# Kernel optimization log

Hardware: AMD Instinct MI355X
Metric: run time of the kernel (lower is better)

## Reference

```python
import jax, jax.numpy as jnp
import numpy as np
import math

# init kwargs (constants)
HSHIFT, VSHIFT, ANGLE = 2, 2, 2
BS, C, H, W = 2048, 1, 64, 64


def setup_inputs() -> dict:
    key = jax.random.key(0)
    k1, k2 = jax.random.split(key)
    fm1 = jax.random.normal(k1, (BS, C, H, W), dtype=jnp.float32)
    fm2 = jax.random.normal(k2, (BS, C, H, W), dtype=jnp.float32)
    return {"fm1": fm1, "fm2": fm2}


def _warp_rotate(img, theta_deg, h, w):
    """Equivalent of cv2.warpAffine(img, cv2.getRotationMatrix2D((w/2,h/2), theta, 1)).

    img: [bs, h, w]. Bilinear interpolation, constant-0 border.
    Returns (rotated_img [bs,h,w], rotated_ones_mask [h,w]).
    cv2 inverts the forward map internally; inverse of rotation by theta about
    the center is rotation by -theta about the center.
    """
    t = -theta_deg * (math.pi / 180.0)
    alpha = jnp.cos(t)
    beta = jnp.sin(t)
    cx, cy = w / 2.0, h / 2.0
    ys, xs = jnp.meshgrid(jnp.arange(h, dtype=jnp.float32),
                          jnp.arange(w, dtype=jnp.float32), indexing="ij")
    x_src = alpha * xs + beta * ys + (1.0 - alpha) * cx - beta * cy
    y_src = -beta * xs + alpha * ys + beta * cx + (1.0 - alpha) * cy

    x0 = jnp.floor(x_src)
    y0 = jnp.floor(y_src)
    wx = x_src - x0
    wy = y_src - y0
    x0i = x0.astype(jnp.int32)
    y0i = y0.astype(jnp.int32)

    out = jnp.zeros_like(img)
    msk = jnp.zeros((h, w), img.dtype)
    corners = ((0, 0, (1 - wy) * (1 - wx)), (0, 1, (1 - wy) * wx),
               (1, 0, wy * (1 - wx)), (1, 1, wy * wx))
    for dy, dx, wgt in corners:
        yi = y0i + dy
        xi = x0i + dx
        valid = ((yi >= 0) & (yi < h) & (xi >= 0) & (xi < w)).astype(img.dtype)
        yc = jnp.clip(yi, 0, h - 1)
        xc = jnp.clip(xi, 0, w - 1)
        out = out + (wgt * valid) * img[:, yc, xc]
        msk = msk + wgt * valid
    return out, msk


def _forward(fm1, fm2):
    bs, c, h, w = fm1.shape
    thetas = jnp.arange(-ANGLE, ANGLE + 1, dtype=jnp.float32)
    min_dist = jnp.full((bs,), jnp.finfo(jnp.float32).max, dtype=jnp.float32)
    for bh in range(-HSHIFT, HSHIFT + 1):
        for bv in range(-VSHIFT, VSHIFT + 1):
            if bh >= 0:
                r1, r2 = fm1[:, :, :, :w - bh], fm2[:, :, :, bh:]
            else:
                r1, r2 = fm1[:, :, :, -bh:], fm2[:, :, :, :w + bh]
            if bv >= 0:
                r1, r2 = r1[:, :, :h - bv, :], r2[:, :, bv:, :]
            else:
                r1, r2 = r1[:, :, -bv:, :], r2[:, :, :h + bv, :]
            oh, ow = r1.shape[2], r1.shape[3]
            r1s = r1[:, 0]  # [bs, oh, ow] (C==1)
            # original detaches ref2 before warping (cv2 path)
            r2s = jax.lax.stop_gradient(r2[:, 0])

            def one_theta(theta, r1s=r1s, r2s=r2s, oh=oh, ow=ow):
                rr2, mk = _warp_rotate(r2s, theta, oh, ow)
                se = ((r1s - rr2) ** 2) * mk  # [bs, oh, ow]
                return se.reshape(se.shape[0], -1).sum(1) / mk.sum()

            dists = jax.vmap(one_theta)(thetas)  # [ntheta, bs]
            min_dist = jnp.minimum(min_dist, dists.min(0))
    return min_dist


def reference(fm1, fm2):
    return _forward(fm1, fm2)
```

## Files before the change

kernel.cpp:

```cpp
#include <hip/hip_runtime.h>
#include <hip/hip_fp16.h>
#include <math.h>

#define NTH 5
#define GLO 66
#define GHI 132
#define PS (GLO + 4096 + GHI)

#define ALP0 0.99939082701909576f
#define ALP1 0.99984769515639127f
constexpr float ALPc[5] = {ALP0, ALP1, 1.0f, ALP1, ALP0};
constexpr float BETc[5] = {0.03489949670250097f, 0.01745240643728351f, 0.0f,
                           -0.01745240643728351f, -0.03489949670250097f};

__device__ __forceinline__ unsigned h2bits(float a, float b) {
    __half2 h = __floats2half2_rn(a, b);
    return *(unsigned*)&h;
}
__device__ __forceinline__ __half2 h2(unsigned u) { return *(__half2*)&u; }

__device__ __forceinline__ int pkadd(int a, int b) {
    __half2 r = __hadd2(*(__half2*)&a, *(__half2*)&b);
    return *(int*)&r;
}
__device__ __forceinline__ int hred16(__half2 v) {
    int x = *(int*)&v;
    int t = __builtin_amdgcn_update_dpp(0, x, 0xB1, 0xF, 0xF, true);
    x = pkadd(x, t);
    t = __builtin_amdgcn_update_dpp(0, x, 0x4E, 0xF, 0xF, true);
    x = pkadd(x, t);
    t = __builtin_amdgcn_update_dpp(0, x, 0x141, 0xF, 0xF, true);
    x = pkadd(x, t);
    t = __builtin_amdgcn_update_dpp(0, x, 0x140, 0xF, 0xF, true);
    x = pkadd(x, t);
    return x;
}

__global__ void pack_kernel(const float* __restrict__ fm1,
                            const float* __restrict__ fm2,
                            __half* __restrict__ fm1h,
                            __half* __restrict__ fm2h) {
    const int g = blockIdx.x >> 1;
    const int half = blockIdx.x & 1;
    const int tid = threadIdx.x;
    const size_t inb = (size_t)g * 16 * 4096;
    #pragma unroll
    for (int i = 0; i < 2; i++) {
        const int p = half * 2048 + tid + 1024 * i;
        uint4 wa, wb, va, vb;
        wa.x = h2bits(fm1[inb + 0 * 4096 + p], fm1[inb + 1 * 4096 + p]);
        wa.y = h2bits(fm1[inb + 2 * 4096 + p], fm1[inb + 3 * 4096 + p]);
        wa.z = h2bits(fm1[inb + 4 * 4096 + p], fm1[inb + 5 * 4096 + p]);
        wa.w = h2bits(fm1[inb + 6 * 4096 + p], fm1[inb + 7 * 4096 + p]);
        wb.x = h2bits(fm1[inb + 8 * 4096 + p], fm1[inb + 9 * 4096 + p]);
        wb.y = h2bits(fm1[inb + 10 * 4096 + p], fm1[inb + 11 * 4096 + p]);
        wb.z = h2bits(fm1[inb + 12 * 4096 + p], fm1[inb + 13 * 4096 + p]);
        wb.w = h2bits(fm1[inb + 14 * 4096 + p], fm1[inb + 15 * 4096 + p]);
        va.x = h2bits(fm2[inb + 0 * 4096 + p], fm2[inb + 1 * 4096 + p]);
        va.y = h2bits(fm2[inb + 2 * 4096 + p], fm2[inb + 3 * 4096 + p]);
        va.z = h2bits(fm2[inb + 4 * 4096 + p], fm2[inb + 5 * 4096 + p]);
        va.w = h2bits(fm2[inb + 6 * 4096 + p], fm2[inb + 7 * 4096 + p]);
        vb.x = h2bits(fm2[inb + 8 * 4096 + p], fm2[inb + 9 * 4096 + p]);
        vb.y = h2bits(fm2[inb + 10 * 4096 + p], fm2[inb + 11 * 4096 + p]);
        vb.z = h2bits(fm2[inb + 12 * 4096 + p], fm2[inb + 13 * 4096 + p]);
        vb.w = h2bits(fm2[inb + 14 * 4096 + p], fm2[inb + 15 * 4096 + p]);
        *(uint4*)(fm1h + ((size_t)(g * 2 + 0) * 4096 + p) * 8) = wa;
        *(uint4*)(fm1h + ((size_t)(g * 2 + 1) * 4096 + p) * 8) = wb;
        *(uint4*)(fm2h + ((size_t)(g * 2 + 0) * 4096 + p) * 8) = va;
        *(uint4*)(fm2h + ((size_t)(g * 2 + 1) * 4096 + p) * 8) = vb;
    }
}

__global__ void table_kernel(uint4* __restrict__ tab, float* __restrict__ denom) {
    const int bid = blockIdx.x;
    const int s = bid >> 2, tj = bid & 3;
    const int ti = tj < 2 ? tj : tj + 1;
    const int tid = threadIdx.x;
    const int bh = (s / 5) - 2;
    const int bv = (s % 5) - 2;
    const int ox2 = bh >= 0 ? bh : 0;
    const int ow = 64 - (bh >= 0 ? bh : -bh);
    const int oy2 = bv >= 0 ? bv : 0;
    const int oh = 64 - (bv >= 0 ? bv : -bv);
    const float cx = 0.5f * (float)ow;
    const float cy = 0.5f * (float)oh;
    const float alpha = ALPc[ti], beta = BETc[ti];
    __shared__ float mred[4];
    float macc = 0.0f;
    for (int i = 0; i < 16; i++) {
        const int px = tid + 256 * i;
        const int y = px >> 6, x = px & 63;
        uint4 e = make_uint4(0u, 0u, 0u, (unsigned)GLO);
        if (x < ow && y < oh) {
            const float xs = (float)x, yf = (float)y;
            const float hx = fmaf(alpha, xs, (1.0f - alpha) * cx - beta * cy);
            const float hy = fmaf(-beta, xs, beta * cx + (1.0f - alpha) * cy);
            const float xsrc = fmaf(beta, yf, hx);
            const float ysrc = fmaf(alpha, yf, hy);
            const float x0f = floorf(xsrc), y0f = floorf(ysrc);
            const float wx = xsrc - x0f, wy = ysrc - y0f;
            const int x0 = (int)x0f, y0 = (int)y0f;
            const float ax0 = ((unsigned)x0 < (unsigned)ow) ? (1.f - wx) : 0.f;
            const float ax1 = ((unsigned)(x0 + 1) < (unsigned)ow) ? wx : 0.f;
            const float ay0 = ((unsigned)y0 < (unsigned)oh) ? (1.f - wy) : 0.f;
            const float ay1 = ((unsigned)(y0 + 1) < (unsigned)oh) ? wy : 0.f;
            const int x0c = min(max(x0, -1), ow - 1);
            const int y0c = min(max(y0, -1), oh - 1);
            const float mk = (ax0 + ax1) * (ay0 + ay1);
            e.x = h2bits(ay0 * ax0, ay0 * ax1);
            e.y = h2bits(ay1 * ax0, ay1 * ax1);
            e.z = h2bits(mk, 0.0f);
            e.w = (unsigned)(GLO + (y0c + oy2) * 64 + (x0c + ox2));
            macc += mk;
        }
        tab[(size_t)bid * 4096 + px] = e;
    }
    #pragma unroll
    for (int off = 32; off; off >>= 1) macc += __shfl_xor(macc, off);
    if ((tid & 63) == 0) mred[tid >> 6] = macc;
    __syncthreads();
    if (tid == 0) {
        denom[s * 5 + ti] = mred[0] + mred[1] + mred[2] + mred[3];
        if (tj == 0) denom[s * 5 + 2] = (float)(ow * oh);
    }
}

__launch_bounds__(1024, 8)
__global__ void wrsl_main(const __half* __restrict__ fm1h,
                          const __half* __restrict__ fm2h,
                          const uint4* __restrict__ tab,
                          const float* __restrict__ denom,
                          float* __restrict__ out) {
    __shared__ uint4 lds[PS];
    __shared__ float redm[16][4][40];
    __shared__ float colsum[40];

    const int tid = threadIdx.x;
    const int g = blockIdx.x & 127;
    const int pl = (blockIdx.x >> 7) & 1;
    const int hf = (blockIdx.x >> 8) & 1;
    const int sBeg = hf ? 13 : 0;
    const int sEnd = hf ? 25 : 13;
    const size_t pbase = (size_t)(g * 2 + pl) * 4096;

    {
        const uint4* src = (const uint4*)(fm2h + pbase * 8);
        #pragma unroll
        for (int i = 0; i < 4; i++)
            lds[GLO + tid + 1024 * i] = src[tid + 1024 * i];
        if (tid < GLO + GHI) {
            const int off = (tid < GLO) ? tid : (4096 + tid);
            lds[off] = make_uint4(0u, 0u, 0u, 0u);
        }
    }
    const int lane = tid & 63, wid = tid >> 6;
    __syncthreads();

    float best = 3.4028234663852886e38f;

    for (int s = sBeg; s < sEnd; s++) {
        const int bh = (s / 5) - 2;
        const int bv = (s % 5) - 2;
        const int ox1 = bh >= 0 ? 0 : -bh;
        const int ox2 = bh >= 0 ? bh : 0;
        const int ow = 64 - (bh >= 0 ? bh : -bh);
        const int oy1 = bv >= 0 ? 0 : -bv;
        const int oy2 = bv >= 0 ? bv : 0;
        const int oh = 64 - (bv >= 0 ? bv : -bv);
        const int xcap = ox1 + min(lane, ow - 1);

        uint4 nr[4];
        #pragma unroll
        for (int k = 0; k < 4; k++) {
            const int p1 = (oy1 + min(wid + 16 * k, oh - 1)) * 64 + xcap;
            uint4 a = *(const uint4*)(fm1h + (pbase + p1) * 8);
            a.x ^= 0x80008000u; a.y ^= 0x80008000u; a.z ^= 0x80008000u; a.w ^= 0x80008000u;
            nr[k] = a;
        }

        const uint4* tqbase = tab + (size_t)(s * 4) * 4096;
        uint4 tv[4];
        #pragma unroll
        for (int k = 0; k < 4; k++)
            tv[k] = tqbase[(wid + 16 * k) * 64 + lane];

        {
            const float xinf = (lane < ow) ? 1.0f : 0.0f;
            const __half2 z2 = __float2half2_rn(0.0f);
            __half2 se[4] = {z2, z2, z2, z2};
            #pragma unroll
            for (int k = 0; k < 4; k++) {
                const int y = wid + 16 * k;
                const __half2 msk = __float2half2_rn((y < oh) ? xinf : 0.0f);
                const int idx = GLO + (oy2 + y) * 64 + ox2 + lane;
                const uint4 qa = lds[idx];
                #define LIGHT(SE, C)                                          \
                {                                                             \
                    __half2 d = __hmul2(__hadd2(h2(qa.C), h2(nr[k].C)), msk); \
                    SE = __hfma2(d, d, SE);                                   \
                }
                LIGHT(se[0], x) LIGHT(se[1], y) LIGHT(se[2], z) LIGHT(se[3], w)
                #undef LIGHT
            }
            int r0 = hred16(se[0]), r1 = hred16(se[1]);
            int r2 = hred16(se[2]), r3 = hred16(se[3]);
            if ((lane & 15) == 0) {
                float2 f0 = __half22float2(h2(r0)), f1 = __half22float2(h2(r1));
                float2 f2 = __half22float2(h2(r2)), f3 = __half22float2(h2(r3));
                float4* dst = (float4*)&redm[wid][lane >> 4][2 * 8];
                dst[0] = make_float4(f0.x, f0.y, f1.x, f1.y);
                dst[1] = make_float4(f2.x, f2.y, f3.x, f3.y);
            }
        }

        #pragma unroll
        for (int tj = 0; tj < 4; tj++) {
            const int ti = tj < 2 ? tj : tj + 1;
            uint4 tvn[4];
            if (tj < 3) {
                const uint4* tqn = tqbase + (size_t)(tj + 1) * 4096;
                #pragma unroll
                for (int k = 0; k < 4; k++)
                    tvn[k] = tqn[(wid + 16 * k) * 64 + lane];
            }

            const __half2 z2 = __float2half2_rn(0.0f);
            __half2 se[4] = {z2, z2, z2, z2};
            #pragma unroll
            for (int k = 0; k < 4; k++) {
                const __half2 tx = h2(tv[k].x), ty = h2(tv[k].y);
                const __half2 w00p = __low2half2(tx), w01p = __high2half2(tx);
                const __half2 w10p = __low2half2(ty), w11p = __high2half2(ty);
                const __half2 mkp = __low2half2(h2(tv[k].z));
                const int b0 = (int)tv[k].w;
                const uint4 q00 = lds[b0], q01 = lds[b0 + 1];
                const uint4 q10 = lds[b0 + 64], q11 = lds[b0 + 65];
                #define FULL(SE, C)                                        \
                {                                                          \
                    __half2 r = __hfma2(w00p, h2(q00.C), h2(nr[k].C));     \
                    r = __hfma2(w01p, h2(q01.C), r);                       \
                    r = __hfma2(w10p, h2(q10.C), r);                       \
                    r = __hfma2(w11p, h2(q11.C), r);                       \
                    SE = __hfma2(__hmul2(r, mkp), r, SE);                  \
                }
                FULL(se[0], x) FULL(se[1], y) FULL(se[2], z) FULL(se[3], w)
                #undef FULL
            }
            int r0 = hred16(se[0]), r1 = hred16(se[1]);
            int r2 = hred16(se[2]), r3 = hred16(se[3]);
            if ((lane & 15) == 0) {
                float2 f0 = __half22float2(h2(r0)), f1 = __half22float2(h2(r1));
                float2 f2 = __half22float2(h2(r2)), f3 = __half22float2(h2(r3));
                float4* dst = (float4*)&redm[wid][lane >> 4][ti * 8];
                dst[0] = make_float4(f0.x, f0.y, f1.x, f1.y);
                dst[1] = make_float4(f2.x, f2.y, f3.x, f3.y);
            }
            if (tj < 3) {
                #pragma unroll
                for (int k = 0; k < 4; k++) tv[k] = tvn[k];
            }
        }

        __syncthreads();
        if (tid < 40) {
            float sum = 0.0f;
            #pragma unroll 8
            for (int w = 0; w < 16; w++) {
                sum += redm[w][0][tid] + redm[w][1][tid] + redm[w][2][tid] + redm[w][3][tid];
            }
            colsum[tid] = sum;
        }
        __syncthreads();
        if (tid < 8) {
            #pragma unroll
            for (int t2 = 0; t2 < NTH; t2++)
                best = fminf(best, colsum[t2 * 8 + tid] / denom[s * 5 + t2]);
        }
    }
    if (tid < 8)
        atomicMin((unsigned int*)&out[g * 16 + pl * 8 + tid], __float_as_uint(best));
}

extern "C" void kernel_launch(void* const* d_in, const int* in_sizes, int n_in,
                              void* d_out, int out_size, void* d_ws, size_t ws_size,
                              hipStream_t stream) {
    const float* fm1 = (const float*)d_in[0];
    const float* fm2 = (const float*)d_in[1];
    float* out = (float*)d_out;
    __half* fm1h = (__half*)d_ws;
    __half* fm2h = (__half*)((char*)d_ws + ((size_t)16 << 20));
    uint4* tab = (uint4*)((char*)d_ws + ((size_t)32 << 20));
    float* denom = (float*)((char*)d_ws + ((size_t)32 << 20) + (size_t)100 * 4096 * 16);

    hipMemsetAsync(d_out, 0x7F, (size_t)out_size * 4, stream);
    pack_kernel<<<256, 1024, 0, stream>>>(fm1, fm2, fm1h, fm2h);
    table_kernel<<<100, 256, 0, stream>>>(tab, denom);
    wrsl_main<<<512, 1024, 0, stream>>>(fm1h, fm2h, tab, denom, out);
}
```

Measured before the change: 184.7 us.

## Merge prep kernels, process two shifts per barrier pair, widen DPP reduction

Folds the pack and table kernels into one launch, with table blocks resized to 1024 threads. The main kernel now handles two shift positions between each pair of block barriers, doubling the reduction buffers, so there are fewer __syncthreads. The half-precision DPP reduction adds one row-broadcast step to sum 32 lanes, which halves the shared-memory partial writes. The upper halo shrinks because light-path row indices are now clamped; this saves a little LDS but adds indexing work.

```diff
diff --git a/kernel.cpp b/kernel.cpp
--- a/kernel.cpp
+++ b/kernel.cpp
@@ -4,7 +4,7 @@
 
 #define NTH 5
 #define GLO 66
-#define GHI 132
+#define GHI 66
 #define PS (GLO + 4096 + GHI)
 
 #define ALP0 0.99939082701909576f
@@ -23,7 +23,7 @@
     __half2 r = __hadd2(*(__half2*)&a, *(__half2*)&b);
     return *(int*)&r;
 }
-__device__ __forceinline__ int hred16(__half2 v) {
+__device__ __forceinline__ int hred32(__half2 v) {
     int x = *(int*)&v;
     int t = __builtin_amdgcn_update_dpp(0, x, 0xB1, 0xF, 0xF, true);
     x = pkadd(x, t);
@@ -33,49 +33,53 @@
     x = pkadd(x, t);
     t = __builtin_amdgcn_update_dpp(0, x, 0x140, 0xF, 0xF, true);
     x = pkadd(x, t);
+    t = __builtin_amdgcn_update_dpp(0, x, 0x142, 0xF, 0xF, true);
+    x = pkadd(x, t);
     return x;
 }
 
-__global__ void pack_kernel(const float* __restrict__ fm1,
+__global__ void prep_kernel(const float* __restrict__ fm1,
                             const float* __restrict__ fm2,
                             __half* __restrict__ fm1h,
-                            __half* __restrict__ fm2h) {
-    const int g = blockIdx.x >> 1;
-    const int half = blockIdx.x & 1;
+                            __half* __restrict__ fm2h,
+                            uint4* __restrict__ tab,
+                            float* __restrict__ denom) {
     const int tid = threadIdx.x;
-    const size_t inb = (size_t)g * 16 * 4096;
-    #pragma unroll
-    for (int i = 0; i < 2; i++) {
-        const int p = half * 2048 + tid + 1024 * i;
-        uint4 wa, wb, va, vb;
-        wa.x = h2bits(fm1[inb + 0 * 4096 + p], fm1[inb + 1 * 4096 + p]);
-        wa.y = h2bits(fm1[inb + 2 * 4096 + p], fm1[inb + 3 * 4096 + p]);
-        wa.z = h2bits(fm1[inb + 4 * 4096 + p], fm1[inb + 5 * 4096 + p]);
-        wa.w = h2bits(fm1[inb + 6 * 4096 + p], fm1[inb + 7 * 4096 + p]);
-        wb.x = h2bits(fm1[inb + 8 * 4096 + p], fm1[inb + 9 * 4096 + p]);
-        wb.y = h2bits(fm1[inb + 10 * 4096 + p], fm1[inb + 11 * 4096 + p]);
-        wb.z = h2bits(fm1[inb + 12 * 4096 + p], fm1[inb + 13 * 4096 + p]);
-        wb.w = h2bits(fm1[inb + 14 * 4096 + p], fm1[inb + 15 * 4096 + p]);
-        va.x = h2bits(fm2[inb + 0 * 4096 + p], fm2[inb + 1 * 4096 + p]);
-        va.y = h2bits(fm2[inb + 2 * 4096 + p], fm2[inb + 3 * 4096 + p]);
-        va.z = h2bits(fm2[inb + 4 * 4096 + p], fm2[inb + 5 * 4096 + p]);
-        va.w = h2bits(fm2[inb + 6 * 4096 + p], fm2[inb + 7 * 4096 + p]);
-        vb.x = h2bits(fm2[inb + 8 * 4096 + p], fm2[inb + 9 * 4096 + p]);
-        vb.y = h2bits(fm2[inb + 10 * 4096 + p], fm2[inb + 11 * 4096 + p]);
-        vb.z = h2bits(fm2[inb + 12 * 4096 + p], fm2[inb + 13 * 4096 + p]);
-        vb.w = h2bits(fm2[inb + 14 * 4096 + p], fm2[inb + 15 * 4096 + p]);
-        *(uint4*)(fm1h + ((size_t)(g * 2 + 0) * 4096 + p) * 8) = wa;
-        *(uint4*)(fm1h + ((size_t)(g * 2 + 1) * 4096 + p) * 8) = wb;
-        *(uint4*)(fm2h + ((size_t)(g * 2 + 0) * 4096 + p) * 8) = va;
-        *(uint4*)(fm2h + ((size_t)(g * 2 + 1) * 4096 + p) * 8) = vb;
-    }
-}
-
-__global__ void table_kernel(uint4* __restrict__ tab, float* __restrict__ denom) {
-    const int bid = blockIdx.x;
-    const int s = bid >> 2, tj = bid & 3;
+    if (blockIdx.x < 256) {
+        const int g = blockIdx.x >> 1;
+        const int half = blockIdx.x & 1;
+        const size_t inb = (size_t)g * 16 * 4096;
+        #pragma unroll
+        for (int i = 0; i < 2; i++) {
+            const int p = half * 2048 + tid + 1024 * i;
+            uint4 wa, wb, va, vb;
+            wa.x = h2bits(fm1[inb + 0 * 4096 + p], fm1[inb + 1 * 4096 + p]);
+            wa.y = h2bits(fm1[inb + 2 * 4096 + p], fm1[inb + 3 * 4096 + p]);
+            wa.z = h2bits(fm1[inb + 4 * 4096 + p], fm1[inb + 5 * 4096 + p]);
+            wa.w = h2bits(fm1[inb + 6 * 4096 + p], fm1[inb + 7 * 4096 + p]);
+            wb.x = h2bits(fm1[inb + 8 * 4096 + p], fm1[inb + 9 * 4096 + p]);
+            wb.y = h2bits(fm1[inb + 10 * 4096 + p], fm1[inb + 11 * 4096 + p]);
+            wb.z = h2bits(fm1[inb + 12 * 4096 + p], fm1[inb + 13 * 4096 + p]);
+            wb.w = h2bits(fm1[inb + 14 * 4096 + p], fm1[inb + 15 * 4096 + p]);
+            va.x = h2bits(fm2[inb + 0 * 4096 + p], fm2[inb + 1 * 4096 + p]);
+            va.y = h2bits(fm2[inb + 2 * 4096 + p], fm2[inb + 3 * 4096 + p]);
+            va.z = h2bits(fm2[inb + 4 * 4096 + p], fm2[inb + 5 * 4096 + p]);
+            va.w = h2bits(fm2[inb + 6 * 4096 + p], fm2[inb + 7 * 4096 + p]);
+            vb.x = h2bits(fm2[inb + 8 * 4096 + p], fm2[inb + 9 * 4096 + p]);
+            vb.y = h2bits(fm2[inb + 10 * 4096 + p], fm2[inb + 11 * 4096 + p]);
+            vb.z = h2bits(fm2[inb + 12 * 4096 + p], fm2[inb + 13 * 4096 + p]);
+            vb.w = h2bits(fm2[inb + 14 * 4096 + p], fm2[inb + 15 * 4096 + p]);
+            *(uint4*)(fm1h + ((size_t)(g * 2 + 0) * 4096 + p) * 8) = wa;
+            *(uint4*)(fm1h + ((size_t)(g * 2 + 1) * 4096 + p) * 8) = wb;
+            *(uint4*)(fm2h + ((size_t)(g * 2 + 0) * 4096 + p) * 8) = va;
+            *(uint4*)(fm2h + ((size_t)(g * 2 + 1) * 4096 + p) * 8) = vb;
+        }
+        return;
+    }
+    __shared__ float mred[16];
+    const int tb = blockIdx.x - 256;
+    const int s = tb >> 2, tj = tb & 3;
     const int ti = tj < 2 ? tj : tj + 1;
-    const int tid = threadIdx.x;
     const int bh = (s / 5) - 2;
     const int bv = (s % 5) - 2;
     const int ox2 = bh >= 0 ? bh : 0;
@@ -85,10 +89,10 @@
     const float cx = 0.5f * (float)ow;
     const float cy = 0.5f * (float)oh;
     const float alpha = ALPc[ti], beta = BETc[ti];
-    __shared__ float mred[4];
     float macc = 0.0f;
-    for (int i = 0; i < 16; i++) {
-        const int px = tid + 256 * i;
+    #pragma unroll
+    for (int i = 0; i < 4; i++) {
+        const int px = tid + 1024 * i;
         const int y = px >> 6, x = px & 63;
         uint4 e = make_uint4(0u, 0u, 0u, (unsigned)GLO);
         if (x < ow && y < oh) {
@@ -113,14 +117,17 @@
             e.w = (unsigned)(GLO + (y0c + oy2) * 64 + (x0c + ox2));
             macc += mk;
         }
-        tab[(size_t)bid * 4096 + px] = e;
+        tab[(size_t)tb * 4096 + px] = e;
     }
     #pragma unroll
     for (int off = 32; off; off >>= 1) macc += __shfl_xor(macc, off);
     if ((tid & 63) == 0) mred[tid >> 6] = macc;
     __syncthreads();
     if (tid == 0) {
-        denom[s * 5 + ti] = mred[0] + mred[1] + mred[2] + mred[3];
+        float d = 0.0f;
+        #pragma unroll
+        for (int w = 0; w < 16; w++) d += mred[w];
+        denom[s * 5 + ti] = d;
         if (tj == 0) denom[s * 5 + 2] = (float)(ow * oh);
     }
 }
@@ -132,8 +139,8 @@
                           const float* __restrict__ denom,
                           float* __restrict__ out) {
     __shared__ uint4 lds[PS];
-    __shared__ float redm[16][4][40];
-    __shared__ float colsum[40];
+    __shared__ float redm[2][16][2][40];
+    __shared__ float colsum[80];
 
     const int tid = threadIdx.x;
     const int g = blockIdx.x & 127;
@@ -158,123 +165,131 @@
 
     float best = 3.4028234663852886e38f;
 
-    for (int s = sBeg; s < sEnd; s++) {
-        const int bh = (s / 5) - 2;
-        const int bv = (s % 5) - 2;
-        const int ox1 = bh >= 0 ? 0 : -bh;
-        const int ox2 = bh >= 0 ? bh : 0;
-        const int ow = 64 - (bh >= 0 ? bh : -bh);
-        const int oy1 = bv >= 0 ? 0 : -bv;
-        const int oy2 = bv >= 0 ? bv : 0;
-        const int oh = 64 - (bv >= 0 ? bv : -bv);
-        const int xcap = ox1 + min(lane, ow - 1);
-
-        uint4 nr[4];
-        #pragma unroll
-        for (int k = 0; k < 4; k++) {
-            const int p1 = (oy1 + min(wid + 16 * k, oh - 1)) * 64 + xcap;
-            uint4 a = *(const uint4*)(fm1h + (pbase + p1) * 8);
-            a.x ^= 0x80008000u; a.y ^= 0x80008000u; a.z ^= 0x80008000u; a.w ^= 0x80008000u;
-            nr[k] = a;
-        }
-
-        const uint4* tqbase = tab + (size_t)(s * 4) * 4096;
-        uint4 tv[4];
-        #pragma unroll
-        for (int k = 0; k < 4; k++)
-            tv[k] = tqbase[(wid + 16 * k) * 64 + lane];
-
-        {
-            const float xinf = (lane < ow) ? 1.0f : 0.0f;
-            const __half2 z2 = __float2half2_rn(0.0f);
-            __half2 se[4] = {z2, z2, z2, z2};
+    for (int s0 = sBeg; s0 < sEnd; s0 += 2) {
+        const int nsh = min(2, sEnd - s0);
+        for (int sh = 0; sh < nsh; sh++) {
+            const int s = s0 + sh;
+            const int bh = (s / 5) - 2;
+            const int bv = (s % 5) - 2;
+            const int ox1 = bh >= 0 ? 0 : -bh;
+            const int ox2 = bh >= 0 ? bh : 0;
+            const int ow = 64 - (bh >= 0 ? bh : -bh);
+            const int oy1 = bv >= 0 ? 0 : -bv;
+            const int oy2 = bv >= 0 ? bv : 0;
+            const int oh = 64 - (bv >= 0 ? bv : -bv);
+            const int xcap = ox1 + min(lane, ow - 1);
+
+            uint4 nr[4];
             #pragma unroll
             for (int k = 0; k < 4; k++) {
-                const int y = wid + 16 * k;
-                const __half2 msk = __float2half2_rn((y < oh) ? xinf : 0.0f);
-                const int idx = GLO + (oy2 + y) * 64 + ox2 + lane;
-                const uint4 qa = lds[idx];
-                #define LIGHT(SE, C)                                          \
-                {                                                             \
-                    __half2 d = __hmul2(__hadd2(h2(qa.C), h2(nr[k].C)), msk); \
-                    SE = __hfma2(d, d, SE);                                   \
-                }
-                LIGHT(se[0], x) LIGHT(se[1], y) LIGHT(se[2], z) LIGHT(se[3], w)
-                #undef LIGHT
+                const int p1 = (oy1 + min(wid + 16 * k, oh - 1)) * 64 + xcap;
+                uint4 a = *(const uint4*)(fm1h + (pbase + p1) * 8);
+                a.x ^= 0x80008000u; a.y ^= 0x80008000u;
+                a.z ^= 0x80008000u; a.w ^= 0x80008000u;
+                nr[k] = a;
             }
-            int r0 = hred16(se[0]), r1 = hred16(se[1]);
-            int r2 = hred16(se[2]), r3 = hred16(se[3]);
-            if ((lane & 15) == 0) {
-                float2 f0 = __half22float2(h2(r0)), f1 = __half22float2(h2(r1));
-                float2 f2 = __half22float2(h2(r2)), f3 = __half22float2(h2(r3));
-                float4* dst = (float4*)&redm[wid][lane >> 4][2 * 8];
-                dst[0] = make_float4(f0.x, f0.y, f1.x, f1.y);
-                dst[1] = make_float4(f2.x, f2.y, f3.x, f3.y);
+
+            const uint4* tqbase = tab + (size_t)(s * 4) * 4096;
+            uint4 tv[4];
+            #pragma unroll
+            for (int k = 0; k < 4; k++)
+                tv[k] = tqbase[(wid + 16 * k) * 64 + lane];
+
+            {
+                const float xinf = (lane < ow) ? 1.0f : 0.0f;
+                const __half2 z2 = __float2half2_rn(0.0f);
+                __half2 se[4] = {z2, z2, z2, z2};
+                #pragma unroll
+                for (int k = 0; k < 4; k++) {
+                    const int y = wid + 16 * k;
+                    const __half2 msk = __float2half2_rn((y < oh) ? xinf : 0.0f);
+                    const int idx = GLO + (oy2 + min(y, oh - 1)) * 64 + ox2 + lane;
+                    const uint4 qa = lds[idx];
+                    #define LIGHT(SE, C)                                          \
+                    {                                                             \
+                        __half2 d = __hmul2(__hadd2(h2(qa.C), h2(nr[k].C)), msk); \
+                        SE = __hfma2(d, d, SE);                                   \
+                    }
+                    LIGHT(se[0], x) LIGHT(se[1], y) LIGHT(se[2], z) LIGHT(se[3], w)
+                    #undef LIGHT
+                }
+                int r0 = hred32(se[0]), r1 = hred32(se[1]);
+                int r2 = hred32(se[2]), r3 = hred32(se[3]);
+                if ((lane & 31) == 16) {
+                    float2 f0 = __half22float2(h2(r0)), f1 = __half22float2(h2(r1));
+                    float2 f2 = __half22float2(h2(r2)), f3 = __half22float2(h2(r3));
+                    float4* dst = (float4*)&redm[sh][wid][lane >> 5][2 * 8];
+                    dst[0] = make_float4(f0.x, f0.y, f1.x, f1.y);
+                    dst[1] = make_float4(f2.x, f2.y, f3.x, f3.y);
+                }
             }
-        }
-
-        #pragma unroll
-        for (int tj = 0; tj < 4; tj++) {
-            const int ti = tj < 2 ? tj : tj + 1;
-            uint4 tvn[4];
-            if (tj < 3) {
-                const uint4* tqn = tqbase + (size_t)(tj + 1) * 4096;
+
+            #pragma unroll
+            for (int tj = 0; tj < 4; tj++) {
+                const int ti = tj < 2 ? tj : tj + 1;
+                uint4 tvn[4];
+                if (tj < 3) {
+                    const uint4* tqn = tqbase + (size_t)(tj + 1) * 4096;
+                    #pragma unroll
+                    for (int k = 0; k < 4; k++)
+                        tvn[k] = tqn[(wid + 16 * k) * 64 + lane];
+                }
+
+                const __half2 z2 = __float2half2_rn(0.0f);
+                __half2 se[4] = {z2, z2, z2, z2};
                 #pragma unroll
-                for (int k = 0; k < 4; k++)
-                    tvn[k] = tqn[(wid + 16 * k) * 64 + lane];
+                for (int k = 0; k < 4; k++) {
+                    const __half2 tx = h2(tv[k].x), ty = h2(tv[k].y);
+                    const __half2 w00p = __low2half2(tx), w01p = __high2half2(tx);
+                    const __half2 w10p = __low2half2(ty), w11p = __high2half2(ty);
+                    const __half2 mkp = __low2half2(h2(tv[k].z));
+                    const int b0 = (int)tv[k].w;
+                    const uint4 q00 = lds[b0], q01 = lds[b0 + 1];
+                    const uint4 q10 = lds[b0 + 64], q11 = lds[b0 + 65];
+                    #define FULL(SE, C)                                        \
+                    {                                                          \
+                        __half2 r = __hfma2(w00p, h2(q00.C), h2(nr[k].C));     \
+                        r = __hfma2(w01p, h2(q01.C), r);                       \
+                        r = __hfma2(w10p, h2(q10.C), r);                       \
+                        r = __hfma2(w11p, h2(q11.C), r);                       \
+                        SE = __hfma2(__hmul2(r, mkp), r, SE);                  \
+                    }
+                    FULL(se[0], x) FULL(se[1], y) FULL(se[2], z) FULL(se[3], w)
+                    #undef FULL
+                }
+                int r0 = hred32(se[0]), r1 = hred32(se[1]);
+                int r2 = hred32(se[2]), r3 = hred32(se[3]);
+                if ((lane & 31) == 16) {
+                    float2 f0 = __half22float2(h2(r0)), f1 = __half22float2(h2(r1));
+                    float2 f2 = __half22float2(h2(r2)), f3 = __half22float2(h2(r3));
+                    float4* dst = (float4*)&redm[sh][wid][lane >> 5][ti * 8];
+                    dst[0] = make_float4(f0.x, f0.y, f1.x, f1.y);
+                    dst[1] = make_float4(f2.x, f2.y, f3.x, f3.y);
+                }
+                if (tj < 3) {
+                    #pragma unroll
+                    for (int k = 0; k < 4; k++) tv[k] = tvn[k];
+                }
             }
-
-            const __half2 z2 = __float2half2_rn(0.0f);
-            __half2 se[4] = {z2, z2, z2, z2};
-            #pragma unroll
-            for (int k = 0; k < 4; k++) {
-                const __half2 tx = h2(tv[k].x), ty = h2(tv[k].y);
-                const __half2 w00p = __low2half2(tx), w01p = __high2half2(tx);
-                const __half2 w10p = __low2half2(ty), w11p = __high2half2(ty);
-                const __half2 mkp = __low2half2(h2(tv[k].z));
-                const int b0 = (int)tv[k].w;
-                const uint4 q00 = lds[b0], q01 = lds[b0 + 1];
-                const uint4 q10 = lds[b0 + 64], q11 = lds[b0 + 65];
-                #define FULL(SE, C)                                        \
-                {                                                          \
-                    __half2 r = __hfma2(w00p, h2(q00.C), h2(nr[k].C));     \
-                    r = __hfma2(w01p, h2(q01.C), r);                       \
-                    r = __hfma2(w10p, h2(q10.C), r);                       \
-                    r = __hfma2(w11p, h2(q11.C), r);                       \
-                    SE = __hfma2(__hmul2(r, mkp), r, SE);                  \
-                }
-                FULL(se[0], x) FULL(se[1], y) FULL(se[2], z) FULL(se[3], w)
-                #undef FULL
-            }
-            int r0 = hred16(se[0]), r1 = hred16(se[1]);
-            int r2 = hred16(se[2]), r3 = hred16(se[3]);
-            if ((lane & 15) == 0) {
-                float2 f0 = __half22float2(h2(r0)), f1 = __half22float2(h2(r1));
-                float2 f2 = __half22float2(h2(r2)), f3 = __half22float2(h2(r3));
-                float4* dst = (float4*)&redm[wid][lane >> 4][ti * 8];
-                dst[0] = make_float4(f0.x, f0.y, f1.x, f1.y);
-                dst[1] = make_float4(f2.x, f2.y, f3.x, f3.y);
-            }
-            if (tj < 3) {
-                #pragma unroll
-                for (int k = 0; k < 4; k++) tv[k] = tvn[k];
-            }
         }
 
         __syncthreads();
-        if (tid < 40) {
+        if (tid < nsh * 40) {
+            const int sh = tid / 40, c = tid - sh * 40;
             float sum = 0.0f;
             #pragma unroll 8
-            for (int w = 0; w < 16; w++) {
-                sum += redm[w][0][tid] + redm[w][1][tid] + redm[w][2][tid] + redm[w][3][tid];
-            }
-            colsum[tid] = sum;
+            for (int w = 0; w < 16; w++)
+                sum += redm[sh][w][0][c] + redm[sh][w][1][c];
+            colsum[sh * 40 + c] = sum;
         }
         __syncthreads();
         if (tid < 8) {
-            #pragma unroll
-            for (int t2 = 0; t2 < NTH; t2++)
-                best = fminf(best, colsum[t2 * 8 + tid] / denom[s * 5 + t2]);
+            for (int sh = 0; sh < nsh; sh++) {
+                #pragma unroll
+                for (int t2 = 0; t2 < NTH; t2++)
+                    best = fminf(best,
+                                 colsum[sh * 40 + t2 * 8 + tid] / denom[(s0 + sh) * 5 + t2]);
+            }
         }
     }
     if (tid < 8)
@@ -293,7 +308,6 @@
     float* denom = (float*)((char*)d_ws + ((size_t)32 << 20) + (size_t)100 * 4096 * 16);
 
     hipMemsetAsync(d_out, 0x7F, (size_t)out_size * 4, stream);
-    pack_kernel<<<256, 1024, 0, stream>>>(fm1, fm2, fm1h, fm2h);
-    table_kernel<<<100, 256, 0, stream>>>(tab, denom);
+    prep_kernel<<<356, 1024, 0, stream>>>(fm1, fm2, fm1h, fm2h, tab, denom);
     wrsl_main<<<512, 1024, 0, stream>>>(fm1h, fm2h, tab, denom, out);
 }
```

Result: no change. 186.1 us (+0.8%).
